# Optimization experiments

Measured on AMD Instinct MI355X. Metric: run time of the kernel, lower is better.

## Reference

```python
import jax, jax.numpy as jnp
import numpy as np
from jax import lax

C = 128      # channels
H = 128
W = 128
B = 2
WS = 4       # window size
HEADS = 4
HID = int(C * 2.66)  # 340
EPS = 1e-6


def conv1x1(x, w):
    # x: [b,c,h,w], w: [out,in]
    return jnp.einsum('oc,bchw->bohw', w, x)


def dwconv3(x, w):
    # depthwise 3x3, w: [c,1,3,3]
    return lax.conv_general_dilated(
        x, w, window_strides=(1, 1), padding='SAME',
        feature_group_count=x.shape[1],
        dimension_numbers=('NCHW', 'OIHW', 'NCHW'))


def layernorm(x, w, b):
    # channel-wise LN over dim 1 (per pixel), w/b: [C]
    m = x.mean(axis=1, keepdims=True)
    v = ((x - m) ** 2).mean(axis=1, keepdims=True)
    xn = (x - m) / jnp.sqrt(v + EPS)
    return xn * w[None, :, None, None] + b[None, :, None, None]


def l2norm(x):
    n = jnp.sqrt(jnp.sum(x * x, axis=-1, keepdims=True))
    return x / jnp.maximum(n, 1e-12)


def rsa(x, qkv_w, dw_w, proj_w, temp):
    b, c, h, w = x.shape
    ws = WS
    x_ = jnp.roll(x, (-ws // 2, -ws // 2), axis=(2, 3))  # shifts > 0
    qkv = dwconv3(conv1x1(x_, qkv_w), dw_w)
    q, k, v = jnp.split(qkv, 3, axis=1)

    def win(t):  # b c (h dh) (w dw) -> b (h w) (dh dw) c
        return t.reshape(b, c, h // ws, ws, w // ws, ws) \
                .transpose(0, 2, 4, 3, 5, 1) \
                .reshape(b, (h // ws) * (w // ws), ws * ws, c)

    q, k, v = win(q), win(k), win(v)
    q = l2norm(q)
    k = l2norm(k)
    # attn = q^T @ k  -> [b, nw, c, c]
    attn = jax.nn.relu(jnp.einsum('bnpc,bnpd->bncd', q, k) * temp[0, 0, 0])
    out = jnp.einsum('bnpc,bncd->bnpd', v, attn)  # v @ attn
    out = out.reshape(b, h // ws, w // ws, ws, ws, c) \
             .transpose(0, 5, 1, 3, 2, 4).reshape(b, c, h, w)
    out = jnp.roll(out, (ws // 2, ws // 2), axis=(2, 3))
    return conv1x1(out, proj_w)


def gsa(x, qkv_w, dw_w, proj_w, temp):
    b, c, h, w = x.shape
    hd = HEADS
    ch = c // hd
    qkv = dwconv3(conv1x1(x, qkv_w), dw_w)
    q, k, v = jnp.split(qkv, 3, axis=1)

    def hs(t):  # b (head c) h w -> b head c (h w)
        return t.reshape(b, hd, ch, h * w)

    q, k, v = hs(q), hs(k), hs(v)
    q = l2norm(q)
    k = l2norm(k)
    attn = jax.nn.relu(jnp.einsum('bhcn,bhdn->bhcd', q, k) * temp[0, 0, 0])
    out = jnp.einsum('bhcd,bhdn->bhcn', attn, v).reshape(b, c, h, w)
    return conv1x1(out, proj_w)


def ffn(x, w_in, w_dw, w_out):
    h = dwconv3(conv1x1(x, w_in), w_dw)
    h = jax.nn.gelu(h, approximate=False)
    return conv1x1(h, w_out)


def setup_inputs() -> dict:
    key = jax.random.key(0)
    ks = jax.random.split(key, 16)
    s = 0.05
    d = {
        'x': jax.random.normal(ks[0], (B, C, H, W), jnp.float32),
        # spatial (RSA) branch
        'w_s0': jnp.ones((C,), jnp.float32), 'b_s0': jnp.zeros((C,), jnp.float32),
        'w_s2': jnp.ones((C,), jnp.float32), 'b_s2': jnp.zeros((C,), jnp.float32),
        'rsa_qkv': jax.random.normal(ks[1], (3 * C, C), jnp.float32) * s,
        'rsa_dw': jax.random.normal(ks[2], (3 * C, 1, 3, 3), jnp.float32) * s,
        'rsa_proj': jax.random.normal(ks[3], (C, C), jnp.float32) * s,
        'rsa_temp': jnp.ones((1, 1, 1), jnp.float32),
        'ffs_in': jax.random.normal(ks[4], (HID, C), jnp.float32) * s,
        'ffs_dw': jax.random.normal(ks[5], (HID, 1, 3, 3), jnp.float32) * s,
        'ffs_out': jax.random.normal(ks[6], (C, HID), jnp.float32) * s,
        # channel (GSA) branch
        'w_c0': jnp.ones((C,), jnp.float32), 'b_c0': jnp.zeros((C,), jnp.float32),
        'w_c2': jnp.ones((C,), jnp.float32), 'b_c2': jnp.zeros((C,), jnp.float32),
        'gsa_qkv': jax.random.normal(ks[7], (3 * C, C), jnp.float32) * s,
        'gsa_dw': jax.random.normal(ks[8], (3 * C, 1, 3, 3), jnp.float32) * s,
        'gsa_proj': jax.random.normal(ks[9], (C, C), jnp.float32) * s,
        'gsa_temp': jnp.ones((1, 1, 1), jnp.float32),
        'ffc_in': jax.random.normal(ks[10], (HID, C), jnp.float32) * s,
        'ffc_dw': jax.random.normal(ks[11], (HID, 1, 3, 3), jnp.float32) * s,
        'ffc_out': jax.random.normal(ks[12], (C, HID), jnp.float32) * s,
    }
    return d


def reference(x, w_s0, b_s0, w_s2, b_s2, rsa_qkv, rsa_dw, rsa_proj, rsa_temp,
              ffs_in, ffs_dw, ffs_out,
              w_c0, b_c0, w_c2, b_c2, gsa_qkv, gsa_dw, gsa_proj, gsa_temp,
              ffc_in, ffc_dw, ffc_out):
    # shared_depth = 1: only the i==0 branches execute
    # spatial block (RSA)
    x_ = rsa(layernorm(x, w_s0, b_s0), rsa_qkv, rsa_dw, rsa_proj, rsa_temp)
    x = ffn(layernorm(x_ + x, w_s2, b_s2), ffs_in, ffs_dw, ffs_out) + x_
    # channel block (GSA)
    x_ = gsa(layernorm(x, w_c0, b_c0), gsa_qkv, gsa_dw, gsa_proj, gsa_temp)
    x = ffn(layernorm(x_ + x, w_c2, b_c2), ffc_in, ffc_dw, ffc_out) + x_
    return x
```

## Files before the change

### kernel.cpp

```cpp
#include <hip/hip_runtime.h>
#include <hip/hip_bf16.h>
#include <math.h>

typedef __hip_bfloat16 bf16;
typedef __attribute__((ext_vector_type(8))) short short8;
typedef __attribute__((ext_vector_type(4))) short short4v;
typedef __attribute__((ext_vector_type(4))) float float4v;

static constexpr int cB  = 2;
static constexpr int cC  = 128;
static constexpr int cH  = 128;
static constexpr int cW  = 128;
static constexpr int cP  = cH * cW;
static constexpr int cC3 = 384;
static constexpr int cHID = 340;
static constexpr int cNW = 1024;
static constexpr float cEPS = 1e-6f;

__device__ __forceinline__ float bfu2f(unsigned short u){
  union { unsigned int i; float f; } c; c.i = ((unsigned int)u) << 16; return c.f;
}
__device__ __forceinline__ unsigned short f2b(float f){
  union { float f; unsigned int u; } c; c.f = f;
  unsigned int r = c.u + 0x7FFFu + ((c.u >> 16) & 1u);
  return (unsigned short)(r >> 16);
}

__global__ void k_wcvt(const float* __restrict__ qkv_s, const float* __restrict__ qkv_c,
                       const float* __restrict__ fin_s, const float* __restrict__ fin_c,
                       const float* __restrict__ prj_s, const float* __restrict__ prj_c,
                       const float* __restrict__ fo_s,  const float* __restrict__ fo_c,
                       unsigned short* __restrict__ WB, float* __restrict__ S){
  int i = blockIdx.x * 256 + threadIdx.x;
  if (i >= 319488){
    int j = i - 319488;
    if (j < 8704) S[j] = 0.f;
    return;
  }
  float v;
  if (i < 98304){
    v = (i < 49152) ? qkv_s[i] : qkv_c[i - 49152];
  } else if (i < 196608){
    int j = (i < 147456) ? (i - 98304) : (i - 147456);
    int row = j >> 7, col = j & 127;
    const float* src = (i < 147456) ? fin_s : fin_c;
    v = (row < cHID) ? src[row * 128 + col] : 0.f;
  } else if (i < 229376){
    v = (i < 212992) ? prj_s[i - 196608] : prj_c[i - 212992];
  } else {
    int j = (i < 274432) ? (i - 229376) : (i - 274432);
    int row = j / 352, col = j - row * 352;
    const float* src = (i < 274432) ? fo_s : fo_c;
    v = (col < cHID) ? src[row * cHID + col] : 0.f;
  }
  WB[i] = f2b(v);
}

__global__ void __launch_bounds__(256) k_gemmLN(const unsigned short* __restrict__ Wb,
                                                const float* __restrict__ Xf,
                                                const float* __restrict__ gamma,
                                                const float* __restrict__ beta,
                                                unsigned short* __restrict__ Out){
  __shared__ short Xls[64 * 136];
  __shared__ short Wls[128 * 40];
  __shared__ float gls[128], bls[128];
  __shared__ float psum[64], pssq[64];
  int bid = blockIdx.x;
  int s  = (bid & 7) * 192 + (bid >> 3);
  int mt = s % 3;
  int r3 = s / 3;
  int pt = r3 & 255;
  int b  = r3 >> 8;
  int p0 = pt * 64;
  int m0 = mt * 128;
  int t  = threadIdx.x;
  int px = t & 63, cq = t >> 6;
  if (t < 64){ psum[t] = 0.f; pssq[t] = 0.f; }
  if (t < 128){ gls[t] = gamma[t]; bls[t] = beta[t]; }
  int rh = p0 >> 7, w0 = p0 & 127;
  int hs = (rh + 2) & (cH - 1);
  int sp = hs * cW + ((w0 + 2 + px) & (cW - 1));
  const float* xb = Xf + (size_t)b * cC * cP + sp;
  float xr[32];
  float s1 = 0.f, s2 = 0.f;
  #pragma unroll
  for (int j = 0; j < 32; j++){
    float v = xb[(size_t)(cq * 32 + j) * cP];
    xr[j] = v; s1 += v; s2 += v * v;
  }
  __syncthreads();
  atomicAdd(&psum[px], s1);
  atomicAdd(&pssq[px], s2);
  __syncthreads();
  float mean = psum[px] * (1.f / cC);
  float var  = pssq[px] * (1.f / cC) - mean * mean;
  float rstd = rsqrtf(var + cEPS);
  #pragma unroll
  for (int k = 0; k < 4; k++){
    short8 tv;
    #pragma unroll
    for (int e = 0; e < 8; e++){
      int c = cq * 32 + k * 8 + e;
      tv[e] = (short)f2b((xr[k * 8 + e] - mean) * rstd * gls[c] + bls[c]);
    }
    *(short8*)&Xls[px * 136 + cq * 32 + k * 8] = tv;
  }
  int lanelo = t & 15;
  int quad   = (t >> 4) & 3;
  int wv = t >> 6;
  int w1 = wv & 1;
  int w2 = wv >> 1;
  int srw = t >> 1;
  int kow = (t & 1) * 16;
  float4v acc[2][4];
  #pragma unroll
  for (int i = 0; i < 2; i++)
    #pragma unroll
    for (int j = 0; j < 4; j++)
      acc[i][j] = (float4v){0.f, 0.f, 0.f, 0.f};
  const unsigned short* Wp = Wb + (size_t)(m0 + srw) * 128 + kow;
  short8 a0 = *(const short8*)(Wp);
  short8 a1 = *(const short8*)(Wp + 8);
  for (int k0 = 0; k0 < 128; k0 += 32){
    __syncthreads();
    *(short8*)&Wls[srw * 40 + kow]     = a0;
    *(short8*)&Wls[srw * 40 + kow + 8] = a1;
    __syncthreads();
    if (k0 < 96){
      a0 = *(const short8*)(Wp + k0 + 32);
      a1 = *(const short8*)(Wp + k0 + 40);
    }
    short8 af[2], bfr[4];
    #pragma unroll
    for (int i = 0; i < 2; i++)
      af[i] = *(const short8*)&Xls[(w1 * 32 + i * 16 + lanelo) * 136 + k0 + quad * 8];
    #pragma unroll
    for (int j = 0; j < 4; j++)
      bfr[j] = *(const short8*)&Wls[(w2 * 64 + j * 16 + lanelo) * 40 + quad * 8];
    #pragma unroll
    for (int i = 0; i < 2; i++)
      #pragma unroll
      for (int j = 0; j < 4; j++)
        acc[i][j] = __builtin_amdgcn_mfma_f32_16x16x32_bf16(af[i], bfr[j], acc[i][j], 0, 0, 0);
  }
  __syncthreads();
  #pragma unroll
  for (int i = 0; i < 2; i++)
    #pragma unroll
    for (int j = 0; j < 4; j++){
      int pixloc = w1 * 32 + i * 16 + quad * 4;
      int mloc   = w2 * 64 + j * 16 + lanelo;
      #pragma unroll
      for (int r = 0; r < 4; r++)
        Xls[(pixloc + r) * 136 + mloc] = (short)f2b(acc[i][j][r]);
    }
  __syncthreads();
  unsigned short* Ob = Out + (size_t)b * cP * cC3;
  #pragma unroll
  for (int rr = 0; rr < 4; rr++){
    int id = t + rr * 256;
    int row = id >> 4, col8 = (id & 15) * 8;
    *(short8*)(Ob + (size_t)(p0 + row) * cC3 + m0 + col8) = *(const short8*)&Xls[row * 136 + col8];
  }
}

__global__ void __launch_bounds__(256) k_gemm(const unsigned short* __restrict__ Wb,
                                              const unsigned short* __restrict__ Xg,
                                              unsigned short* __restrict__ Out,
                                              int K, int PK, int PM){
  __shared__ short SMEM[8704];
  short* Wls = SMEM;
  short* Xls = SMEM + 5120;
  int bid = blockIdx.x;
  int s  = (bid & 7) * (1536 >> 3) + (bid >> 3);
  int mt = s % 3;
  int r3 = s / 3;
  int pt = r3 & 255;
  int b  = r3 >> 8;
  int p0 = pt * 64;
  int m0 = mt * 128;
  int t  = threadIdx.x;
  int lanelo = t & 15;
  int quad   = (t >> 4) & 3;
  int wv = t >> 6;
  int w1 = wv & 1;
  int w2 = wv >> 1;
  int srw = t >> 1;
  int kow = (t & 1) * 16;
  int srx = t >> 2;
  int kox = (t & 3) * 8;

  float4v acc[2][4];
  #pragma unroll
  for (int i = 0; i < 2; i++)
    #pragma unroll
    for (int j = 0; j < 4; j++)
      acc[i][j] = (float4v){0.f, 0.f, 0.f, 0.f};

  const unsigned short* Xp = Xg + (size_t)b * cP * PK + (size_t)(p0 + srx) * PK + kox;
  const unsigned short* Wp = Wb + (size_t)(m0 + srw) * K + kow;

  short8 xv  = *(const short8*)(Xp);
  short8 wv0 = *(const short8*)(Wp);
  short8 wv1 = *(const short8*)(Wp + 8);
  for (int k0 = 0; k0 < K; k0 += 32){
    __syncthreads();
    *(short8*)&Wls[srw * 40 + kow]     = wv0;
    *(short8*)&Wls[srw * 40 + kow + 8] = wv1;
    *(short8*)&Xls[srx * 40 + kox]     = xv;
    __syncthreads();
    if (k0 + 32 < K){
      xv  = *(const short8*)(Xp + k0 + 32);
      wv0 = *(const short8*)(Wp + k0 + 32);
      wv1 = *(const short8*)(Wp + k0 + 40);
    }
    short8 af[2], bfr[4];
    #pragma unroll
    for (int i = 0; i < 2; i++)
      af[i] = *(const short8*)&Xls[(w1 * 32 + i * 16 + lanelo) * 40 + quad * 8];
    #pragma unroll
    for (int j = 0; j < 4; j++)
      bfr[j] = *(const short8*)&Wls[(w2 * 64 + j * 16 + lanelo) * 40 + quad * 8];
    #pragma unroll
    for (int i = 0; i < 2; i++)
      #pragma unroll
      for (int j = 0; j < 4; j++)
        acc[i][j] = __builtin_amdgcn_mfma_f32_16x16x32_bf16(af[i], bfr[j], acc[i][j], 0, 0, 0);
  }
  __syncthreads();
  #pragma unroll
  for (int i = 0; i < 2; i++)
    #pragma unroll
    for (int j = 0; j < 4; j++){
      int pixloc = w1 * 32 + i * 16 + quad * 4;
      int mloc   = w2 * 64 + j * 16 + lanelo;
      #pragma unroll
      for (int r = 0; r < 4; r++)
        SMEM[(pixloc + r) * 136 + mloc] = (short)f2b(acc[i][j][r]);
    }
  __syncthreads();
  unsigned short* Ob = Out + (size_t)b * cP * PM;
  #pragma unroll
  for (int rr = 0; rr < 4; rr++){
    int id = t + rr * 256;
    int row = id >> 4, col8 = (id & 15) * 8;
    int wcol = m0 + col8;
    if (wcol < PM)
      *(short8*)(Ob + (size_t)(p0 + row) * PM + wcol) = *(const short8*)&SMEM[row * 136 + col8];
  }
}

template<int MODE>
__global__ void __launch_bounds__(256) k_gemm64(const unsigned short* __restrict__ Wb,
                                                const unsigned short* __restrict__ Xg,
                                                const float* __restrict__ R,
                                                const float* __restrict__ Base,
                                                const float* __restrict__ gamma,
                                                const float* __restrict__ beta,
                                                float* __restrict__ Tr,
                                                unsigned short* __restrict__ LNo,
                                                int K, int PK){
  __shared__ short SMEM[8704];
  __shared__ float gls[128], bls[128];
  __shared__ float psum[64], pssq[64];
  short* Wls = SMEM;
  short* Xls = SMEM + 5120;
  int b  = blockIdx.z;
  int p0 = blockIdx.x * 64;
  int t  = threadIdx.x;
  int lanelo = t & 15;
  int quad   = (t >> 4) & 3;
  int wv = t >> 6;
  int w2 = wv >> 1, w1 = wv & 1;
  int srw = t >> 1;
  int kow = (t & 1) * 16;
  int srx = t >> 2;
  int kox = (t & 3) * 8;

  if (MODE != 3){
    if (t < 128){ gls[t] = gamma[t]; bls[t] = beta[t]; }
    if (t < 64){ psum[t] = 0.f; pssq[t] = 0.f; }
  }

  float4v acc[4][2];
  #pragma unroll
  for (int i = 0; i < 4; i++){
    acc[i][0] = (float4v){0.f, 0.f, 0.f, 0.f};
    acc[i][1] = (float4v){0.f, 0.f, 0.f, 0.f};
  }
  const unsigned short* Xp = Xg + (size_t)b * cP * PK + (size_t)(p0 + srx) * PK + kox;
  const unsigned short* Wp = Wb + (size_t)srw * K + kow;

  short8 xv  = *(const short8*)(Xp);
  short8 wv0 = *(const short8*)(Wp);
  short8 wv1 = *(const short8*)(Wp + 8);
  for (int k0 = 0; k0 < K; k0 += 32){
    __syncthreads();
    *(short8*)&Wls[srw * 40 + kow]     = wv0;
    *(short8*)&Wls[srw * 40 + kow + 8] = wv1;
    *(short8*)&Xls[srx * 40 + kox]     = xv;
    __syncthreads();
    if (k0 + 32 < K){
      xv  = *(const short8*)(Xp + k0 + 32);
      wv0 = *(const short8*)(Wp + k0 + 32);
      wv1 = *(const short8*)(Wp + k0 + 40);
    }
    short8 af[4], bfr[2];
    #pragma unroll
    for (int i = 0; i < 4; i++)
      af[i] = *(const short8*)&Wls[(w2 * 64 + i * 16 + lanelo) * 40 + quad * 8];
    #pragma unroll
    for (int j = 0; j < 2; j++)
      bfr[j] = *(const short8*)&Xls[(w1 * 32 + j * 16 + lanelo) * 40 + quad * 8];
    #pragma unroll
    for (int i = 0; i < 4; i++)
      #pragma unroll
      for (int j = 0; j < 2; j++)
        acc[i][j] = __builtin_amdgcn_mfma_f32_16x16x32_bf16(af[i], bfr[j], acc[i][j], 0, 0, 0);
  }
  float lnv[4][2][4];
  #pragma unroll
  for (int i = 0; i < 4; i++)
    #pragma unroll
    for (int j = 0; j < 2; j++){
      int n = p0 + w1 * 32 + j * 16 + lanelo;
      #pragma unroll
      for (int r = 0; r < 4; r++){
        int m = w2 * 64 + i * 16 + quad * 4 + r;
        size_t idx = (size_t)b * cC * cP + (size_t)m * cP + n;
        float v = acc[i][j][r];
        if (MODE >= 2) v += R[idx];
        Tr[idx] = v;
        if (MODE == 1) v += Base[idx];
        lnv[i][j][r] = v;
      }
    }
  if (MODE == 3) return;
  __syncthreads();
  #pragma unroll
  for (int j = 0; j < 2; j++){
    int nl = w1 * 32 + j * 16 + lanelo;
    float s = 0.f, ss = 0.f;
    #pragma unroll
    for (int i = 0; i < 4; i++)
      #pragma unroll
      for (int r = 0; r < 4; r++){
        float v = lnv[i][j][r];
        s += v; ss += v * v;
      }
    atomicAdd(&psum[nl], s);
    atomicAdd(&pssq[nl], ss);
  }
  __syncthreads();
  #pragma unroll
  for (int j = 0; j < 2; j++){
    int nl = w1 * 32 + j * 16 + lanelo;
    float mean = psum[nl] * (1.f / cC);
    float var = pssq[nl] * (1.f / cC) - mean * mean;
    float rstd = rsqrtf(var + cEPS);
    #pragma unroll
    for (int i = 0; i < 4; i++)
      #pragma unroll
      for (int r = 0; r < 4; r++){
        int m = w2 * 64 + i * 16 + quad * 4 + r;
        SMEM[nl * 136 + m] = (short)f2b((lnv[i][j][r] - mean) * rstd * gls[m] + bls[m]);
      }
  }
  __syncthreads();
  unsigned short* Ob = LNo + (size_t)b * cP * cC;
  #pragma unroll
  for (int rr = 0; rr < 4; rr++){
    int id = t + rr * 256;
    int row = id >> 4, col8 = (id & 15) * 8;
    short8 sv = *(const short8*)&SMEM[row * 136 + col8];
    *(short8*)(Ob + (size_t)(p0 + row) * cC + col8) = sv;
  }
}

template<int GELU, int CCn, int PITCH>
__global__ void __launch_bounds__(256) k_dw(const unsigned short* __restrict__ in,
                                            const float* __restrict__ wt,
                                            unsigned short* __restrict__ out){
  __shared__ float wls[16 * 76];
  int t = threadIdx.x;
  int cbase = blockIdx.y * 128;
  for (int i = t; i < 16 * 72; i += 256){
    int cg = i / 72, rem = i - cg * 72;
    int tap = rem >> 3, j = rem & 7;
    int c = cbase + cg * 8 + j;
    wls[cg * 76 + rem] = (c < CCn) ? wt[c * 9 + tap] : 0.f;
  }
  __syncthreads();
  int cgl = t & 15, pixl = t >> 4;
  int c0 = cbase + cgl * 8;
  if (c0 >= PITCH) return;
  int p = blockIdx.x * 16 + pixl;
  int h = p >> 7, w = p & 127;
  int b = blockIdx.z;
  const unsigned short* ib = in + (size_t)b * cP * PITCH;
  float4 wreg[18];
  #pragma unroll
  for (int q = 0; q < 18; q++)
    wreg[q] = *(const float4*)&wls[cgl * 76 + q * 4];
  short8 v[9];
  #pragma unroll
  for (int ky = 0; ky < 3; ky++){
    int hh = h + ky - 1;
    bool okh = (unsigned)hh < (unsigned)cH;
    int hc = okh ? hh : h;
    #pragma unroll
    for (int kx = 0; kx < 3; kx++){
      int ww = w + kx - 1;
      bool okw = (unsigned)ww < (unsigned)cW;
      int wc = okw ? ww : w;
      short8 lv = *(const short8*)(ib + (size_t)(hc * cW + wc) * PITCH + c0);
      if (!(okh && okw)) lv = (short8){0,0,0,0,0,0,0,0};
      v[ky * 3 + kx] = lv;
    }
  }
  float acc[8] = {0,0,0,0,0,0,0,0};
  #pragma unroll
  for (int tap = 0; tap < 9; tap++){
    float4 w0 = wreg[tap * 2];
    float4 w1 = wreg[tap * 2 + 1];
    float wa[8] = {w0.x, w0.y, w0.z, w0.w, w1.x, w1.y, w1.z, w1.w};
    #pragma unroll
    for (int j = 0; j < 8; j++)
      acc[j] += wa[j] * bfu2f((unsigned short)v[tap][j]);
  }
  short8 ov;
  #pragma unroll
  for (int j = 0; j < 8; j++){
    float vv = acc[j];
    if (GELU) vv = 0.5f * vv * (1.f + erff(vv * 0.70710678118654752f));
    ov[j] = (short)f2b(vv);
  }
  *(short8*)(out + (size_t)b * cP * PITCH + (size_t)p * PITCH + c0) = ov;
}

__global__ void __launch_bounds__(256) k_rsa(const unsigned short* __restrict__ qkv,
                                             const float* __restrict__ temp,
                                             unsigned short* __restrict__ out){
  constexpr int QT = 0;
  constexpr int KT = 5120;
  constexpr int VO = 10240;
  constexpr int AT = 12416;
  __shared__ short lds[21632];
  __shared__ float nq[16], nk[16];
  int blk = blockIdx.x;
  int b  = blk >> 10;
  int nw = blk & 1023;
  int hb = nw >> 5, wb = nw & 31;
  int t = threadIdx.x;
  #pragma unroll
  for (int j = 0; j < 5; j++)
    *(short8*)&lds[t * 40 + j * 8] = (short8){0,0,0,0,0,0,0,0};
  if (t < 16) nq[t] = 0.f;
  else if (t < 32) nk[t - 16] = 0.f;
  __syncthreads();
  const unsigned short* base = qkv + (size_t)b * cP * cC3;
  #pragma unroll
  for (int r = 0; r < 3; r++){
    int i = t + 256 * r;
    int pix = i / 48;
    int cg = i - pix * 48;
    int c0 = cg * 8;
    int gp = (hb * 4 + (pix >> 2)) * cW + wb * 4 + (pix & 3);
    short8 v = *(const short8*)(base + (size_t)gp * cC3 + c0);
    if (c0 < 256){
      float s = 0.f;
      #pragma unroll
      for (int e = 0; e < 8; e++){ float f = bfu2f((unsigned short)v[e]); s += f * f; }
      int off = (c0 < 128) ? (QT + c0 * 40) : (KT + (c0 - 128) * 40);
      #pragma unroll
      for (int e = 0; e < 8; e++) lds[off + e * 40 + pix] = v[e];
      atomicAdd((c0 < 128) ? &nq[pix] : &nk[pix], s);
    } else {
      *(short8*)&lds[VO + pix * 136 + (c0 - 256)] = v;
    }
  }
  __syncthreads();
  float T = temp[0];
  #pragma unroll
  for (int r = 0; r < 8; r++){
    int idx = t + 256 * r;
    int c = idx >> 4, p = idx & 15;
    float sc = (1.f / fmaxf(sqrtf(nq[p]), 1e-12f)) * (1.f / fmaxf(sqrtf(nk[p]), 1e-12f));
    int a = QT + c * 40 + p;
    lds[a] = (short)f2b(bfu2f((unsigned short)lds[a]) * sc);
  }
  __syncthreads();
  int lanelo = t & 15;
  int quad = (t >> 4) & 3;
  int wv = t >> 6;
  float4v oacc[2];
  oacc[0] = (float4v){0.f,0.f,0.f,0.f};
  oacc[1] = (float4v){0.f,0.f,0.f,0.f};
  for (int ch = 0; ch < 2; ch++){
    #pragma unroll
    for (int ct = 0; ct < 4; ct++){
      int c0 = ch * 64 + ct * 16;
      short8 af = *(const short8*)&lds[QT + (c0 + lanelo) * 40 + quad * 8];
      #pragma unroll
      for (int dt = 0; dt < 2; dt++){
        int d0 = wv * 32 + dt * 16;
        short8 bf = *(const short8*)&lds[KT + (d0 + lanelo) * 40 + quad * 8];
        float4v acc = __builtin_amdgcn_mfma_f32_16x16x32_bf16(af, bf,
                        (float4v){0.f,0.f,0.f,0.f}, 0, 0, 0);
        short4v sv;
        #pragma unroll
        for (int r2 = 0; r2 < 4; r2++) sv[r2] = (short)f2b(fmaxf(acc[r2] * T, 0.f));
        *(short4v*)&lds[AT + (d0 + lanelo) * 72 + ct * 16 + quad * 4] = sv;
      }
    }
    __syncthreads();
    #pragma unroll
    for (int dt = 0; dt < 2; dt++){
      int d0 = wv * 32 + dt * 16;
      #pragma unroll
      for (int kk = 0; kk < 2; kk++){
        short8 av8 = *(const short8*)&lds[VO + lanelo * 136 + ch * 64 + kk * 32 + quad * 8];
        short8 bv8 = *(const short8*)&lds[AT + (d0 + lanelo) * 72 + kk * 32 + quad * 8];
        oacc[dt] = __builtin_amdgcn_mfma_f32_16x16x32_bf16(av8, bv8, oacc[dt], 0, 0, 0);
      }
    }
    __syncthreads();
  }
  #pragma unroll
  for (int dt = 0; dt < 2; dt++){
    int d = wv * 32 + dt * 16 + lanelo;
    #pragma unroll
    for (int r2 = 0; r2 < 4; r2++){
      int p = quad * 4 + r2;
      lds[p * 136 + d] = (short)f2b(oacc[dt][r2]);
    }
  }
  __syncthreads();
  {
    int px = t >> 4, cg = (t & 15) * 8;
    int h2 = (hb * 4 + (px >> 2) + 2) & (cH - 1);
    int w2 = (wb * 4 + (px & 3) + 2) & (cW - 1);
    short8 sv = *(const short8*)&lds[px * 136 + cg];
    *(short8*)(out + (size_t)b * cP * cC + (size_t)(h2 * cW + w2) * cC + cg) = sv;
  }
}

__global__ void __launch_bounds__(256) k_gram(const unsigned short* __restrict__ qkv,
                                              float* __restrict__ S,
                                              float* __restrict__ Qn,
                                              float* __restrict__ Kn){
  __shared__ float qs[32][132];
  __shared__ float ks[32][132];
  int blk = blockIdx.x;
  int chunk = blk & 127;
  int bh = blk >> 7;
  int b = bh >> 2, hd = bh & 3;
  int n0 = chunk * 128;
  int t = threadIdx.x;
  {
    int row = t >> 1;
    int half = t & 1;
    const unsigned short* pq = qkv + (size_t)b * cP * cC3 + (size_t)(n0 + row) * cC3 + hd * 32 + half * 16;
    const unsigned short* pk = pq + 128;
    short8 q0 = *(const short8*)pq;
    short8 q1 = *(const short8*)(pq + 8);
    short8 k0 = *(const short8*)pk;
    short8 k1 = *(const short8*)(pk + 8);
    #pragma unroll
    for (int e = 0; e < 8; e++){
      qs[half * 16 + e][row]     = bfu2f((unsigned short)q0[e]);
      qs[half * 16 + 8 + e][row] = bfu2f((unsigned short)q1[e]);
      ks[half * 16 + e][row]     = bfu2f((unsigned short)k0[e]);
      ks[half * 16 + 8 + e][row] = bfu2f((unsigned short)k1[e]);
    }
  }
  __syncthreads();
  if (t < 64){
    const float* row = (t < 32) ? qs[t] : ks[t - 32];
    float s = 0.f;
    #pragma unroll
    for (int i = 0; i < 128; i += 4){
      float4 v = *(const float4*)(row + i);
      s += v.x*v.x + v.y*v.y + v.z*v.z + v.w*v.w;
    }
    if (t < 32) atomicAdd(&Qn[bh * 32 + t], s);
    else        atomicAdd(&Kn[bh * 32 + (t - 32)], s);
  }
  int cc = (t >> 4) * 2;
  int dd = t & 15;
  float a00 = 0.f, a01 = 0.f, a10 = 0.f, a11 = 0.f;
  for (int n = 0; n < 128; n += 4){
    float4 q0 = *(const float4*)&qs[cc][n];
    float4 q1 = *(const float4*)&qs[cc + 1][n];
    float4 k0 = *(const float4*)&ks[dd][n];
    float4 k1 = *(const float4*)&ks[dd + 16][n];
    a00 += q0.x*k0.x + q0.y*k0.y + q0.z*k0.z + q0.w*k0.w;
    a01 += q0.x*k1.x + q0.y*k1.y + q0.z*k1.z + q0.w*k1.w;
    a10 += q1.x*k0.x + q1.y*k0.y + q1.z*k0.z + q1.w*k0.w;
    a11 += q1.x*k1.x + q1.y*k1.y + q1.z*k1.z + q1.w*k1.w;
  }
  float* Sb = S + (size_t)bh * 1024;
  atomicAdd(&Sb[cc * 32 + dd], a00);
  atomicAdd(&Sb[cc * 32 + dd + 16], a01);
  atomicAdd(&Sb[(cc + 1) * 32 + dd], a10);
  atomicAdd(&Sb[(cc + 1) * 32 + dd + 16], a11);
}

__global__ void __launch_bounds__(256) k_applyM(const unsigned short* __restrict__ qkv,
                                                const float* __restrict__ S,
                                                const float* __restrict__ Qn,
                                                const float* __restrict__ Kn,
                                                const float* __restrict__ temp,
                                                unsigned short* __restrict__ out){
  __shared__ short atb[128 * 40];
  __shared__ short OT[64 * 136];
  int b = blockIdx.y;
  int nbase = blockIdx.x * 64;
  int t = threadIdx.x;
  float T = temp[0];
  #pragma unroll
  for (int it = 0; it < 16; it++){
    int i = t + it * 256;
    int c = i >> 5, d = i & 31;
    int hd = c >> 5, cl = c & 31;
    int bh = b * 4 + hd;
    float nqv = fmaxf(sqrtf(Qn[bh * 32 + cl]), 1e-12f);
    float nkv = fmaxf(sqrtf(Kn[bh * 32 + d]), 1e-12f);
    float v = fmaxf(S[(size_t)bh * 1024 + cl * 32 + d] / (nqv * nkv) * T, 0.f);
    atb[c * 40 + d] = (short)f2b(v);
  }
  __syncthreads();
  int lanelo = t & 15, quad = (t >> 4) & 3, wv = t >> 6;
  int n0 = nbase + wv * 16;
  const unsigned short* vb = qkv + (size_t)b * cP * cC3 + (size_t)(n0 + lanelo) * cC3 + 256 + quad * 8;
  #pragma unroll
  for (int hd = 0; hd < 4; hd++){
    short8 af = *(const short8*)(vb + hd * 32);
    #pragma unroll
    for (int cth = 0; cth < 2; cth++){
      int c0 = hd * 32 + cth * 16;
      short8 bf = *(const short8*)&atb[(c0 + lanelo) * 40 + quad * 8];
      float4v acc = __builtin_amdgcn_mfma_f32_16x16x32_bf16(af, bf,
                      (float4v){0.f,0.f,0.f,0.f}, 0, 0, 0);
      #pragma unroll
      for (int r = 0; r < 4; r++)
        OT[(wv * 16 + quad * 4 + r) * 136 + c0 + lanelo] = (short)f2b(acc[r]);
    }
  }
  __syncthreads();
  unsigned short* ob = out + (size_t)b * cP * cC;
  #pragma unroll
  for (int rr = 0; rr < 4; rr++){
    int id = t + rr * 256;
    int row = id >> 4, col8 = (id & 15) * 8;
    *(short8*)(ob + (size_t)(nbase + row) * cC + col8) = *(const short8*)&OT[row * 136 + col8];
  }
}

extern "C" void kernel_launch(void* const* d_in, const int* in_sizes, int n_in,
                              void* d_out, int out_size, void* d_ws, size_t ws_size,
                              hipStream_t stream){
  const float* x     = (const float*)d_in[0];
  const float* w_s0  = (const float*)d_in[1];
  const float* b_s0  = (const float*)d_in[2];
  const float* w_s2  = (const float*)d_in[3];
  const float* b_s2  = (const float*)d_in[4];
  const float* rsa_qkv  = (const float*)d_in[5];
  const float* rsa_dw   = (const float*)d_in[6];
  const float* rsa_proj = (const float*)d_in[7];
  const float* rsa_temp = (const float*)d_in[8];
  const float* ffs_in   = (const float*)d_in[9];
  const float* ffs_dw   = (const float*)d_in[10];
  const float* ffs_out  = (const float*)d_in[11];
  const float* w_c0  = (const float*)d_in[12];
  const float* b_c0  = (const float*)d_in[13];
  const float* w_c2  = (const float*)d_in[14];
  const float* b_c2  = (const float*)d_in[15];
  const float* gsa_qkv  = (const float*)d_in[16];
  const float* gsa_dw   = (const float*)d_in[17];
  const float* gsa_proj = (const float*)d_in[18];
  const float* gsa_temp = (const float*)d_in[19];
  const float* ffc_in   = (const float*)d_in[20];
  const float* ffc_dw   = (const float*)d_in[21];
  const float* ffc_out  = (const float*)d_in[22];

  const size_t szC  = (size_t)cB * cC * cP;
  const size_t szC3 = (size_t)cB * cC3 * cP;
  float* XF = (float*)d_ws;
  float* XS = XF + szC;
  unsigned short* LO   = (unsigned short*)(XS + szC);
  unsigned short* Abuf = LO + szC;
  unsigned short* Bbuf = Abuf + szC3;
  float* S  = (float*)(Bbuf + szC3);
  float* Qn = S + 8192;
  float* Kn = Qn + 256;
  float* AT = Kn + 256;
  unsigned short* WB = (unsigned short*)(AT + 1024);
  unsigned short* W_QKV_S = WB;
  unsigned short* W_QKV_C = WB + 49152;
  unsigned short* W_FIN_S = WB + 98304;
  unsigned short* W_FIN_C = WB + 147456;
  unsigned short* W_PRJ_S = WB + 196608;
  unsigned short* W_PRJ_C = WB + 212992;
  unsigned short* W_FO_S  = WB + 229376;
  unsigned short* W_FO_C  = WB + 274432;

  dim3 t256(256);
  dim3 gG1(cP / 64 * 3 * cB);
  dim3 gG64(cP / 64, 1, cB);
  dim3 gDW(cP / 16, 3, cB);

  k_wcvt<<<dim3(1282), t256, 0, stream>>>(rsa_qkv, gsa_qkv, ffs_in, ffc_in,
                                          rsa_proj, gsa_proj, ffs_out, ffc_out, WB, S);

  k_gemmLN<<<gG1, t256, 0, stream>>>(W_QKV_S, x, w_s0, b_s0, Abuf);
  k_dw<0,384,384><<<gDW, t256, 0, stream>>>(Abuf, rsa_dw, Bbuf);
  k_rsa<<<dim3(cB * cNW), t256, 0, stream>>>(Bbuf, rsa_temp, LO);
  k_gemm64<1><<<gG64, t256, 0, stream>>>(W_PRJ_S, LO, nullptr, x, w_s2, b_s2, XS, LO, 128, 128);
  k_gemm<<<gG1, t256, 0, stream>>>(W_FIN_S, LO, Abuf, 128, 128, 352);
  k_dw<1,340,352><<<gDW, t256, 0, stream>>>(Abuf, ffs_dw, Bbuf);
  k_gemm64<2><<<gG64, t256, 0, stream>>>(W_FO_S, Bbuf, XS, nullptr, w_c0, b_c0, XF, LO, 352, 352);

  k_gemm<<<gG1, t256, 0, stream>>>(W_QKV_C, LO, Abuf, 128, 128, 384);
  k_dw<0,384,384><<<gDW, t256, 0, stream>>>(Abuf, gsa_dw, Bbuf);
  k_gram<<<dim3(1024), t256, 0, stream>>>(Bbuf, S, Qn, Kn);
  k_applyM<<<dim3(cP / 64, cB), t256, 0, stream>>>(Bbuf, S, Qn, Kn, gsa_temp, LO);
  k_gemm64<1><<<gG64, t256, 0, stream>>>(W_PRJ_C, LO, nullptr, XF, w_c2, b_c2, XS, LO, 128, 128);
  k_gemm<<<gG1, t256, 0, stream>>>(W_FIN_C, LO, Abuf, 128, 128, 352);
  k_dw<1,340,352><<<gDW, t256, 0, stream>>>(Abuf, ffc_dw, Bbuf);
  k_gemm64<3><<<gG64, t256, 0, stream>>>(W_FO_C, Bbuf, XS, nullptr, nullptr, nullptr,
                                         (float*)d_out, nullptr, 352, 352);
}
```

Baseline: 349.3 us.

## Fuse RSA depthwise 3x3 conv into the window attention kernel

Removes the separate depthwise-conv launch for the RSA qkv tensor. The attention kernel now loads a 6x6 haloed tile of the pre-dwconv qkv into LDS, computes the 3x3 depthwise conv per window, and writes the q, k, v layouts plus norms directly. This saves a full write and re-read of the 384-channel intermediate. In exchange it adds halo reloads (36 vs 16 pixels per window), more LDS per block, and large per-thread weight arrays that may raise register pressure. The haloed tile is read from unshifted coordinates while the reference rolls the input before the qkv conv, so the border semantics need checking.

```diff
diff --git a/kernel.cpp b/kernel.cpp
--- a/kernel.cpp
+++ b/kernel.cpp
@@ -438,14 +438,16 @@
   *(short8*)(out + (size_t)b * cP * PITCH + (size_t)p * PITCH + c0) = ov;
 }
 
-__global__ void __launch_bounds__(256) k_rsa(const unsigned short* __restrict__ qkv,
-                                             const float* __restrict__ temp,
-                                             unsigned short* __restrict__ out){
+__global__ void __launch_bounds__(256) k_rsadw(const unsigned short* __restrict__ qkv,
+                                               const float* __restrict__ wt,
+                                               const float* __restrict__ temp,
+                                               unsigned short* __restrict__ out){
   constexpr int QT = 0;
   constexpr int KT = 5120;
   constexpr int VO = 10240;
+  constexpr int HA = 12416;
   constexpr int AT = 12416;
-  __shared__ short lds[21632];
+  __shared__ short lds[26528];
   __shared__ float nq[16], nk[16];
   int blk = blockIdx.x;
   int b  = blk >> 10;
@@ -460,23 +462,64 @@
   __syncthreads();
   const unsigned short* base = qkv + (size_t)b * cP * cC3;
   #pragma unroll
-  for (int r = 0; r < 3; r++){
+  for (int r = 0; r < 7; r++){
     int i = t + 256 * r;
-    int pix = i / 48;
-    int cg = i - pix * 48;
-    int c0 = cg * 8;
-    int gp = (hb * 4 + (pix >> 2)) * cW + wb * 4 + (pix & 3);
-    short8 v = *(const short8*)(base + (size_t)gp * cC3 + c0);
-    if (c0 < 256){
-      float s = 0.f;
-      #pragma unroll
-      for (int e = 0; e < 8; e++){ float f = bfu2f((unsigned short)v[e]); s += f * f; }
-      int off = (c0 < 128) ? (QT + c0 * 40) : (KT + (c0 - 128) * 40);
-      #pragma unroll
-      for (int e = 0; e < 8; e++) lds[off + e * 40 + pix] = v[e];
-      atomicAdd((c0 < 128) ? &nq[pix] : &nk[pix], s);
-    } else {
-      *(short8*)&lds[VO + pix * 136 + (c0 - 256)] = v;
+    if (i < 1728){
+      int pix6 = i / 48;
+      int cg = i - pix6 * 48;
+      int hy = pix6 / 6, wx = pix6 - hy * 6;
+      int hh = hb * 4 + hy - 1;
+      int ww = wb * 4 + wx - 1;
+      short8 v = (short8){0,0,0,0,0,0,0,0};
+      if ((unsigned)hh < (unsigned)cH && (unsigned)ww < (unsigned)cW)
+        v = *(const short8*)(base + (size_t)(hh * cW + ww) * cC3 + cg * 8);
+      *(short8*)&lds[HA + pix6 * 392 + cg * 8] = v;
+    }
+  }
+  __syncthreads();
+  {
+    int px = t & 15, grp = t >> 4;
+    int py = px >> 2, pw = px & 3;
+    #pragma unroll
+    for (int g = 0; g < 3; g++){
+      int c0 = grp * 24 + g * 8;
+      const float4* wq = (const float4*)(wt + (size_t)c0 * 9);
+      float wa[72];
+      #pragma unroll
+      for (int q = 0; q < 18; q++){
+        float4 v4 = wq[q];
+        wa[q * 4 + 0] = v4.x; wa[q * 4 + 1] = v4.y;
+        wa[q * 4 + 2] = v4.z; wa[q * 4 + 3] = v4.w;
+      }
+      float acc8[8] = {0,0,0,0,0,0,0,0};
+      #pragma unroll
+      for (int ky = 0; ky < 3; ky++)
+        #pragma unroll
+        for (int kx = 0; kx < 3; kx++){
+          short8 iv = *(const short8*)&lds[HA + ((py + ky) * 6 + pw + kx) * 392 + c0];
+          int tap = ky * 3 + kx;
+          #pragma unroll
+          for (int e = 0; e < 8; e++)
+            acc8[e] += wa[e * 9 + tap] * bfu2f((unsigned short)iv[e]);
+        }
+      if (c0 < 256){
+        int isQ = c0 < 128;
+        int off = isQ ? (QT + c0 * 40) : (KT + (c0 - 128) * 40);
+        float s = 0.f;
+        #pragma unroll
+        for (int e = 0; e < 8; e++){
+          unsigned short us = f2b(acc8[e]);
+          float f = bfu2f(us);
+          s += f * f;
+          lds[off + e * 40 + px] = (short)us;
+        }
+        atomicAdd(isQ ? &nq[px] : &nk[px], s);
+      } else {
+        short8 sv;
+        #pragma unroll
+        for (int e = 0; e < 8; e++) sv[e] = (short)f2b(acc8[e]);
+        *(short8*)&lds[VO + px * 136 + (c0 - 256)] = sv;
+      }
     }
   }
   __syncthreads();
@@ -714,8 +757,7 @@
                                           rsa_proj, gsa_proj, ffs_out, ffc_out, WB, S);
 
   k_gemmLN<<<gG1, t256, 0, stream>>>(W_QKV_S, x, w_s0, b_s0, Abuf);
-  k_dw<0,384,384><<<gDW, t256, 0, stream>>>(Abuf, rsa_dw, Bbuf);
-  k_rsa<<<dim3(cB * cNW), t256, 0, stream>>>(Bbuf, rsa_temp, LO);
+  k_rsadw<<<dim3(cB * cNW), t256, 0, stream>>>(Abuf, rsa_dw, rsa_temp, LO);
   k_gemm64<1><<<gG64, t256, 0, stream>>>(W_PRJ_S, LO, nullptr, x, w_s2, b_s2, XS, LO, 128, 128);
   k_gemm<<<gG1, t256, 0, stream>>>(W_FIN_S, LO, Abuf, 128, 128, 352);
   k_dw<1,340,352><<<gDW, t256, 0, stream>>>(Abuf, ffs_dw, Bbuf);
```

Result: faster. 332.9 us (-4.7%).
